# Performance work log

Hardware: AMD Instinct MI355X
Metric: run time of the kernel (lower is better)

Reference implementation:

```python
import jax, jax.numpy as jnp
import numpy as np

N = 500_000        # batch rows
K_OLD = 128        # old bins -> 129 edges
K_NEW = 100        # new bins -> 101 edges


def setup_inputs() -> dict:
    key = jax.random.key(0)
    logits = jax.random.normal(key, (N, K_OLD), dtype=jnp.float32)
    # strictly increasing edge grids (monotone, mismatched resolution)
    old_edges = jnp.linspace(0.0, 1.0, K_OLD + 1, dtype=jnp.float32)
    new_edges = jnp.linspace(0.0, 1.0, K_NEW + 1, dtype=jnp.float32)
    return {"logits": logits, "old_edges": old_edges, "new_edges": new_edges}


def reference(logits, old_edges, new_edges):
    # softmax over bins -> per-bin probability mass
    probs = jax.nn.softmax(logits, axis=-1)                      # [N, K_old]
    widths = old_edges[1:] - old_edges[:-1]                      # [K_old]
    density = probs / widths                                     # [N, K_old]
    # overlap[i, j] = length of intersection of old bin i with new bin j.
    # Equivalent to the per-new-bin mask/gather/sum loop in _rebin_pc:
    # bins with no strict overlap contribute exactly 0 after the clip.
    overlap = jnp.clip(
        jnp.minimum(old_edges[1:, None], new_edges[None, 1:])
        - jnp.maximum(old_edges[:-1, None], new_edges[None, :-1]),
        0.0,
    )                                                            # [K_old, K_new]
    rebinned = density @ overlap                                 # [N, K_new]
    eps = jnp.finfo(rebinned.dtype).tiny
    return jnp.log(rebinned + eps)
```

## Files before the change

### kernel.cpp

```cpp
#include <hip/hip_runtime.h>
#include <math.h>

#define KOLD 128
#define KNEW 100

#define META_OFF 1024
#define PE_OFF   2688
#define LDS_BYTES (PE_OFF + 4 * 4 * 128 * 8)

__launch_bounds__(256, 8)
__global__ void rebin_k(const float* __restrict__ logits,
                        const float* __restrict__ oe,
                        const float* __restrict__ ne,
                        float* __restrict__ out, int nrows)
{
    __shared__ __align__(16) char lds[LDS_BYTES];
    int*   tmp_i = (int*)(lds + 0);
    float* tmp_t = (float*)(lds + 512);
    uint4* meta  = (uint4*)(lds + META_OFF);

    const int tid  = threadIdx.x;
    const int lane = tid & 63;
    const int wid  = tid >> 6;
    const int c    = lane & 31;
    const int half = lane >> 5;

    if (tid <= KNEW) {
        float e = ne[tid];
        int i = 0;
#pragma unroll
        for (int st = 64; st >= 1; st >>= 1) {
            int cand = i + st;
            if (cand <= KOLD - 1 && oe[cand] <= e) i = cand;
        }
        float a = oe[i], b = oe[i + 1];
        float tt = (e - a) / (b - a);
        tmp_i[tid] = i;
        tmp_t[tid] = fminf(fmaxf(tt, 0.f), 1.f);
    }
    __syncthreads();
    if (tid < KNEW) {
        uint4 m;
        m.x = (unsigned)(tmp_i[tid] * 8);
        m.y = __float_as_uint(tmp_t[tid]);
        m.z = (unsigned)(tmp_i[tid + 1] * 8);
        m.w = __float_as_uint(tmp_t[tid + 1]);
        meta[tid] = m;
    }
    __syncthreads();

    const int wrow0 = blockIdx.x * 16 + wid * 4;

    const int nm1 = nrows - 1;
    const size_t offA = (size_t)min(wrow0 + half, nm1) * KOLD + c * 4;
    const size_t offB = (size_t)min(wrow0 + 2 + half, nm1) * KOLD + c * 4;
    const float4 vA = *(const float4*)(logits + offA);
    const float4 vB = *(const float4*)(logits + offB);

    const float eA0 = __expf(fminf(fmaxf(vA.x, -80.f), 80.f));
    const float eA1 = __expf(fminf(fmaxf(vA.y, -80.f), 80.f));
    const float eA2 = __expf(fminf(fmaxf(vA.z, -80.f), 80.f));
    const float eA3 = __expf(fminf(fmaxf(vA.w, -80.f), 80.f));
    const float eB0 = __expf(fminf(fmaxf(vB.x, -80.f), 80.f));
    const float eB1 = __expf(fminf(fmaxf(vB.y, -80.f), 80.f));
    const float eB2 = __expf(fminf(fmaxf(vB.z, -80.f), 80.f));
    const float eB3 = __expf(fminf(fmaxf(vB.w, -80.f), 80.f));

    const float sA = (eA0 + eA1) + (eA2 + eA3);
    const float sB = (eB0 + eB1) + (eB2 + eB3);
    float iA = sA, iB = sB;
#pragma unroll
    for (int off = 1; off <= 16; off <<= 1) {
        float tA = __shfl_up(iA, off, 32);
        float tB = __shfl_up(iB, off, 32);
        if (c >= off) { iA += tA; iB += tB; }
    }
    const float totA = __shfl(iA, 31, 32);
    const float totB = __shfl(iB, 31, 32);
    float rA = __builtin_amdgcn_rcpf(totA);
    float rB = __builtin_amdgcn_rcpf(totB);
    const float invA = rA * (2.0f - totA * rA);
    const float invB = rB * (2.0f - totB * rB);
    const float exA  = iA - sA;
    const float exB  = iB - sB;

    char* peW = lds + PE_OFF + wid * 4096;
    {
        float p0 = exA, p1 = p0 + eA0, p2 = p1 + eA1, p3 = p2 + eA2;
        char* base = peW + half * 1024 + c * 32;
        *(float4*)(base)      = make_float4(eA0 * invA, p0 * invA, eA1 * invA, p1 * invA);
        *(float4*)(base + 16) = make_float4(eA2 * invA, p2 * invA, eA3 * invA, p3 * invA);
    }
    {
        float p0 = exB, p1 = p0 + eB0, p2 = p1 + eB1, p3 = p2 + eB2;
        char* base = peW + (2 + half) * 1024 + c * 32;
        *(float4*)(base)      = make_float4(eB0 * invB, p0 * invB, eB1 * invB, p1 * invB);
        *(float4*)(base + 16) = make_float4(eB2 * invB, p2 * invB, eB3 * invB, p3 * invB);
    }
    asm volatile("s_waitcnt lgkmcnt(0)" ::: "memory");

    const float tiny = 1.1754943508222875e-38f;
    float* gbase = out + (size_t)wrow0 * KNEW;

    if (wrow0 + 16 <= nrows) {
#pragma unroll
        for (int it = 0; it < 7; ++it) {
            const int flat  = it * 64 + lane;
            const int flatc = flat < 399 ? flat : 399;
            const int r = (flatc * 5243) >> 19;
            const int j = flatc - r * 100;
            const uint4 mt = meta[j];
            const char* rowp = peW + r * 1024;
            const float2 ep0 = *(const float2*)(rowp + mt.x);
            const float2 ep1 = *(const float2*)(rowp + mt.z);
            const float F0 = fmaf(__uint_as_float(mt.y), ep0.x, ep0.y);
            const float F1 = fmaf(__uint_as_float(mt.w), ep1.x, ep1.y);
            const float v  = fmaxf(F1 - F0, 0.f) + tiny;
            if (flat < 400) gbase[flat] = __logf(v);
        }
    } else {
        long long liml = (long long)(nrows - wrow0) * KNEW;
        const int lim = liml > 400 ? 400 : (liml < 0 ? 0 : (int)liml);
#pragma unroll
        for (int it = 0; it < 7; ++it) {
            const int flat  = it * 64 + lane;
            const int flatc = flat < 399 ? flat : 399;
            const int r = (flatc * 5243) >> 19;
            const int j = flatc - r * 100;
            const uint4 mt = meta[j];
            const char* rowp = peW + r * 1024;
            const float2 ep0 = *(const float2*)(rowp + mt.x);
            const float2 ep1 = *(const float2*)(rowp + mt.z);
            const float F0 = fmaf(__uint_as_float(mt.y), ep0.x, ep0.y);
            const float F1 = fmaf(__uint_as_float(mt.w), ep1.x, ep1.y);
            const float v  = fmaxf(F1 - F0, 0.f) + tiny;
            if (flat < lim) gbase[flat] = __logf(v);
        }
    }
}

extern "C" void kernel_launch(void* const* d_in, const int* in_sizes, int n_in,
                              void* d_out, int out_size, void* d_ws, size_t ws_size,
                              hipStream_t stream) {
    const float* logits = (const float*)d_in[0];
    const float* oe     = (const float*)d_in[1];
    const float* ne     = (const float*)d_in[2];
    float* out          = (float*)d_out;
    const int nrows     = in_sizes[0] / KOLD;

    const int blocks = (nrows + 15) / 16;
    rebin_k<<<blocks, 256, 0, stream>>>(logits, oe, ne, out, nrows);
}
```

Measured before the change: 97.84 us.

## Process multiple row groups per block and use DPP wave scans

Each block now loops over eight 16-row groups, which spreads the per-block edge-search and metadata setup across more rows and cuts the block count by the same factor. The shuffle-based 32-lane prefix sum is replaced with DPP row-shift adds plus a row_bcast15 step, and the totals are read with readlane. The loop is serial within a wave, so memory latency is less hidden unless the reduced occupancy demand is offset by other resident waves. The per-wave LDS buffer is reused across iterations without an explicit barrier, relying on in-order wave execution.

```diff
diff --git a/kernel.cpp b/kernel.cpp
--- a/kernel.cpp
+++ b/kernel.cpp
@@ -3,10 +3,30 @@
 
 #define KOLD 128
 #define KNEW 100
+#define GPB  8
 
 #define META_OFF 1024
 #define PE_OFF   2688
 #define LDS_BYTES (PE_OFF + 4 * 4 * 128 * 8)
+
+template <int CTRL, int ROWM>
+__device__ __forceinline__ float dpp_add(float v) {
+    int s = __builtin_amdgcn_update_dpp(0, __float_as_int(v), CTRL, ROWM, 0xf, true);
+    return v + __int_as_float(s);
+}
+__device__ __forceinline__ float scan32(float v) {
+    v = dpp_add<0x111, 0xf>(v);
+    v = dpp_add<0x112, 0xf>(v);
+    v = dpp_add<0x114, 0xf>(v);
+    v = dpp_add<0x118, 0xf>(v);
+    v = dpp_add<0x142, 0xa>(v);
+    return v;
+}
+__device__ __forceinline__ float grp_total(float scanned, int half) {
+    int t0 = __builtin_amdgcn_readlane(__float_as_int(scanned), 31);
+    int t1 = __builtin_amdgcn_readlane(__float_as_int(scanned), 63);
+    return __int_as_float(half ? t1 : t0);
+}
 
 __launch_bounds__(256, 8)
 __global__ void rebin_k(const float* __restrict__ logits,
@@ -49,93 +69,95 @@
     }
     __syncthreads();
 
-    const int wrow0 = blockIdx.x * 16 + wid * 4;
+    char* peW = lds + PE_OFF + wid * 4096;
+    const int nm1 = nrows - 1;
+    const int ngroups = (nrows + 15) >> 4;
+    const float tiny = 1.1754943508222875e-38f;
 
-    const int nm1 = nrows - 1;
-    const size_t offA = (size_t)min(wrow0 + half, nm1) * KOLD + c * 4;
-    const size_t offB = (size_t)min(wrow0 + 2 + half, nm1) * KOLD + c * 4;
-    const float4 vA = *(const float4*)(logits + offA);
-    const float4 vB = *(const float4*)(logits + offB);
+#pragma unroll 1
+    for (int k = 0; k < GPB; ++k) {
+        const int grp = blockIdx.x * GPB + k;
+        if (grp >= ngroups) break;
+        const int wrow0 = grp * 16 + wid * 4;
 
-    const float eA0 = __expf(fminf(fmaxf(vA.x, -80.f), 80.f));
-    const float eA1 = __expf(fminf(fmaxf(vA.y, -80.f), 80.f));
-    const float eA2 = __expf(fminf(fmaxf(vA.z, -80.f), 80.f));
-    const float eA3 = __expf(fminf(fmaxf(vA.w, -80.f), 80.f));
-    const float eB0 = __expf(fminf(fmaxf(vB.x, -80.f), 80.f));
-    const float eB1 = __expf(fminf(fmaxf(vB.y, -80.f), 80.f));
-    const float eB2 = __expf(fminf(fmaxf(vB.z, -80.f), 80.f));
-    const float eB3 = __expf(fminf(fmaxf(vB.w, -80.f), 80.f));
+        const size_t offA = (size_t)min(wrow0 + half, nm1) * KOLD + c * 4;
+        const size_t offB = (size_t)min(wrow0 + 2 + half, nm1) * KOLD + c * 4;
+        const float4 vA = *(const float4*)(logits + offA);
+        const float4 vB = *(const float4*)(logits + offB);
 
-    const float sA = (eA0 + eA1) + (eA2 + eA3);
-    const float sB = (eB0 + eB1) + (eB2 + eB3);
-    float iA = sA, iB = sB;
+        const float eA0 = __expf(fminf(fmaxf(vA.x, -80.f), 80.f));
+        const float eA1 = __expf(fminf(fmaxf(vA.y, -80.f), 80.f));
+        const float eA2 = __expf(fminf(fmaxf(vA.z, -80.f), 80.f));
+        const float eA3 = __expf(fminf(fmaxf(vA.w, -80.f), 80.f));
+        const float eB0 = __expf(fminf(fmaxf(vB.x, -80.f), 80.f));
+        const float eB1 = __expf(fminf(fmaxf(vB.y, -80.f), 80.f));
+        const float eB2 = __expf(fminf(fmaxf(vB.z, -80.f), 80.f));
+        const float eB3 = __expf(fminf(fmaxf(vB.w, -80.f), 80.f));
+
+        const float sA = (eA0 + eA1) + (eA2 + eA3);
+        const float sB = (eB0 + eB1) + (eB2 + eB3);
+        const float iA = scan32(sA);
+        const float iB = scan32(sB);
+        const float totA = grp_total(iA, half);
+        const float totB = grp_total(iB, half);
+        float rA = __builtin_amdgcn_rcpf(totA);
+        float rB = __builtin_amdgcn_rcpf(totB);
+        const float invA = rA * (2.0f - totA * rA);
+        const float invB = rB * (2.0f - totB * rB);
+        const float exA  = iA - sA;
+        const float exB  = iB - sB;
+
+        {
+            float p0 = exA, p1 = p0 + eA0, p2 = p1 + eA1, p3 = p2 + eA2;
+            char* base = peW + half * 1024 + c * 32;
+            *(float4*)(base)      = make_float4(eA0 * invA, p0 * invA, eA1 * invA, p1 * invA);
+            *(float4*)(base + 16) = make_float4(eA2 * invA, p2 * invA, eA3 * invA, p3 * invA);
+        }
+        {
+            float p0 = exB, p1 = p0 + eB0, p2 = p1 + eB1, p3 = p2 + eB2;
+            char* base = peW + (2 + half) * 1024 + c * 32;
+            *(float4*)(base)      = make_float4(eB0 * invB, p0 * invB, eB1 * invB, p1 * invB);
+            *(float4*)(base + 16) = make_float4(eB2 * invB, p2 * invB, eB3 * invB, p3 * invB);
+        }
+        asm volatile("s_waitcnt lgkmcnt(0)" ::: "memory");
+
+        float* gbase = out + (size_t)wrow0 * KNEW;
+        if (wrow0 + 4 <= nrows) {
 #pragma unroll
-    for (int off = 1; off <= 16; off <<= 1) {
-        float tA = __shfl_up(iA, off, 32);
-        float tB = __shfl_up(iB, off, 32);
-        if (c >= off) { iA += tA; iB += tB; }
-    }
-    const float totA = __shfl(iA, 31, 32);
-    const float totB = __shfl(iB, 31, 32);
-    float rA = __builtin_amdgcn_rcpf(totA);
-    float rB = __builtin_amdgcn_rcpf(totB);
-    const float invA = rA * (2.0f - totA * rA);
-    const float invB = rB * (2.0f - totB * rB);
-    const float exA  = iA - sA;
-    const float exB  = iB - sB;
-
-    char* peW = lds + PE_OFF + wid * 4096;
-    {
-        float p0 = exA, p1 = p0 + eA0, p2 = p1 + eA1, p3 = p2 + eA2;
-        char* base = peW + half * 1024 + c * 32;
-        *(float4*)(base)      = make_float4(eA0 * invA, p0 * invA, eA1 * invA, p1 * invA);
-        *(float4*)(base + 16) = make_float4(eA2 * invA, p2 * invA, eA3 * invA, p3 * invA);
-    }
-    {
-        float p0 = exB, p1 = p0 + eB0, p2 = p1 + eB1, p3 = p2 + eB2;
-        char* base = peW + (2 + half) * 1024 + c * 32;
-        *(float4*)(base)      = make_float4(eB0 * invB, p0 * invB, eB1 * invB, p1 * invB);
-        *(float4*)(base + 16) = make_float4(eB2 * invB, p2 * invB, eB3 * invB, p3 * invB);
-    }
-    asm volatile("s_waitcnt lgkmcnt(0)" ::: "memory");
-
-    const float tiny = 1.1754943508222875e-38f;
-    float* gbase = out + (size_t)wrow0 * KNEW;
-
-    if (wrow0 + 16 <= nrows) {
+            for (int it = 0; it < 7; ++it) {
+                const int flat  = it * 64 + lane;
+                const int flatc = flat < 399 ? flat : 399;
+                const int r = (flatc * 5243) >> 19;
+                const int j = flatc - r * 100;
+                const uint4 mt = meta[j];
+                const char* rowp = peW + r * 1024;
+                const float2 ep0 = *(const float2*)(rowp + mt.x);
+                const float2 ep1 = *(const float2*)(rowp + mt.z);
+                const float F0 = fmaf(__uint_as_float(mt.y), ep0.x, ep0.y);
+                const float F1 = fmaf(__uint_as_float(mt.w), ep1.x, ep1.y);
+                const float v  = fmaxf(F1 - F0, 0.f) + tiny;
+                if (flat < 400) gbase[flat] = __logf(v);
+            }
+        } else {
+            long long liml = (long long)(nrows - wrow0) * KNEW;
+            const int lim = liml > 400 ? 400 : (liml < 0 ? 0 : (int)liml);
 #pragma unroll
-        for (int it = 0; it < 7; ++it) {
-            const int flat  = it * 64 + lane;
-            const int flatc = flat < 399 ? flat : 399;
-            const int r = (flatc * 5243) >> 19;
-            const int j = flatc - r * 100;
-            const uint4 mt = meta[j];
-            const char* rowp = peW + r * 1024;
-            const float2 ep0 = *(const float2*)(rowp + mt.x);
-            const float2 ep1 = *(const float2*)(rowp + mt.z);
-            const float F0 = fmaf(__uint_as_float(mt.y), ep0.x, ep0.y);
-            const float F1 = fmaf(__uint_as_float(mt.w), ep1.x, ep1.y);
-            const float v  = fmaxf(F1 - F0, 0.f) + tiny;
-            if (flat < 400) gbase[flat] = __logf(v);
+            for (int it = 0; it < 7; ++it) {
+                const int flat  = it * 64 + lane;
+                const int flatc = flat < 399 ? flat : 399;
+                const int r = (flatc * 5243) >> 19;
+                const int j = flatc - r * 100;
+                const uint4 mt = meta[j];
+                const char* rowp = peW + r * 1024;
+                const float2 ep0 = *(const float2*)(rowp + mt.x);
+                const float2 ep1 = *(const float2*)(rowp + mt.z);
+                const float F0 = fmaf(__uint_as_float(mt.y), ep0.x, ep0.y);
+                const float F1 = fmaf(__uint_as_float(mt.w), ep1.x, ep1.y);
+                const float v  = fmaxf(F1 - F0, 0.f) + tiny;
+                if (flat < lim) gbase[flat] = __logf(v);
+            }
         }
-    } else {
-        long long liml = (long long)(nrows - wrow0) * KNEW;
-        const int lim = liml > 400 ? 400 : (liml < 0 ? 0 : (int)liml);
-#pragma unroll
-        for (int it = 0; it < 7; ++it) {
-            const int flat  = it * 64 + lane;
-            const int flatc = flat < 399 ? flat : 399;
-            const int r = (flatc * 5243) >> 19;
-            const int j = flatc - r * 100;
-            const uint4 mt = meta[j];
-            const char* rowp = peW + r * 1024;
-            const float2 ep0 = *(const float2*)(rowp + mt.x);
-            const float2 ep1 = *(const float2*)(rowp + mt.z);
-            const float F0 = fmaf(__uint_as_float(mt.y), ep0.x, ep0.y);
-            const float F1 = fmaf(__uint_as_float(mt.w), ep1.x, ep1.y);
-            const float v  = fmaxf(F1 - F0, 0.f) + tiny;
-            if (flat < lim) gbase[flat] = __logf(v);
-        }
+        asm volatile("" ::: "memory");
     }
 }
 
@@ -148,6 +170,7 @@
     float* out          = (float*)d_out;
     const int nrows     = in_sizes[0] / KOLD;
 
-    const int blocks = (nrows + 15) / 16;
+    const int ngroups = (nrows + 15) / 16;
+    const int blocks  = (ngroups + GPB - 1) / GPB;
     rebin_k<<<blocks, 256, 0, stream>>>(logits, oe, ne, out, nrows);
 }
```

Result: no change. 99.33 us (+1.5%).
